# Optimization experiments

Measured on AMD Instinct MI355X. Metric: run time of the kernel, lower is better.

## Reference

```python
import jax, jax.numpy as jnp
import numpy as np

NHEAD = 16
EPS_L1 = 1e-12
LN_EPS = 1e-5


def _layernorm(x, g, b):
    mu = jnp.mean(x, axis=-1, keepdims=True)
    var = jnp.mean(jnp.square(x - mu), axis=-1, keepdims=True)
    return (x - mu) / jnp.sqrt(var + LN_EPS) * g + b


def setup_inputs() -> dict:
    key = jax.random.key(0)
    ks = jax.random.split(key, 16)
    S, B, E, P, F = 2048, 2, 1024, 64, 4096
    sc = lambda n: 1.0 / np.sqrt(n)
    return {
        "src": jax.random.normal(ks[0], (S, B, E), jnp.float32),
        "pos_embed": jax.random.normal(ks[1], (B, P, S), jnp.float32),
        "in_proj_w": jax.random.normal(ks[2], (3 * E, E), jnp.float32) * sc(E),
        "in_proj_b": jnp.zeros((3 * E,), jnp.float32),
        "out_w": jax.random.normal(ks[3], (E, E), jnp.float32) * sc(E),
        "out_b": jnp.zeros((E,), jnp.float32),
        "lin1_w": jax.random.normal(ks[4], (F, E), jnp.float32) * sc(E),
        "lin1_b": jnp.zeros((F,), jnp.float32),
        "lin2_w": jax.random.normal(ks[5], (E, F), jnp.float32) * sc(F),
        "lin2_b": jnp.zeros((E,), jnp.float32),
        "ln1_g": jnp.ones((E,), jnp.float32),
        "ln1_b": jnp.zeros((E,), jnp.float32),
        "ln2_g": jnp.ones((E,), jnp.float32),
        "ln2_b": jnp.zeros((E,), jnp.float32),
        "pos_w": jax.random.normal(ks[6], (P, P), jnp.float32) * sc(P),
        "pos_b": jnp.zeros((P,), jnp.float32),
    }


def reference(src, pos_embed, in_proj_w, in_proj_b, out_w, out_b,
              lin1_w, lin1_b, lin2_w, lin2_b,
              ln1_g, ln1_b, ln2_g, ln2_b, pos_w, pos_b):
    S, B, E = src.shape
    H = NHEAD
    Dh = E // H

    # --- custom positional-similarity kernel (cosine_similarity w/ L1 norm) ---
    pe = jnp.einsum('bps,qp->bqs', pos_embed, pos_w) + pos_b[None, :, None]  # learnable pos
    l1 = jnp.maximum(jnp.sum(jnp.abs(pe), axis=1, keepdims=True), EPS_L1)
    pe = pe / l1                                                # [B,P,S]
    pos_sim = jnp.einsum('bps,bpt->bst', pe, pe)                # [B,S,S]

    # --- manual multi-head self-attention ---
    qkv = src @ in_proj_w.T + in_proj_b                          # [S,B,3E]
    q, k, v = jnp.split(qkv, 3, axis=-1)
    q = q * (Dh ** -0.5)
    to_bhsd = lambda t: jnp.transpose(t.reshape(S, B, H, Dh), (1, 2, 0, 3))
    q, k, v = to_bhsd(q), to_bhsd(k), to_bhsd(v)                 # [B,H,S,Dh]
    scores = jnp.einsum('bhsd,bhtd->bhst', q, k) + pos_sim[:, None]
    attn = jax.nn.softmax(scores, axis=-1)                       # [B,H,S,S]
    ctx = jnp.einsum('bhst,bhtd->bhsd', attn, v)                 # [B,H,S,Dh]
    ctx = jnp.transpose(ctx, (2, 0, 1, 3)).reshape(S, B, E)
    attn_out = ctx @ out_w.T + out_b

    # --- residual + norm + FFN (post-norm, relu) ---
    x = _layernorm(src + attn_out, ln1_g, ln1_b)
    ff = jax.nn.relu(x @ lin1_w.T + lin1_b) @ lin2_w.T + lin2_b
    return _layernorm(x + ff, ln2_g, ln2_b)
```

## Files before the change

### kernel.cpp

```cpp
#include <hip/hip_runtime.h>
#include <hip/hip_bf16.h>
#include <math.h>

#define S_LEN 2048
#define BATCH 2
#define EMB   1024
#define NH    16
#define DH    64
#define E3    3072
#define FF    4096
#define PP    64
#define QSCALE 0.18033688f
#define LOG2E  1.4426950408889634f

typedef __bf16 bf16x8 __attribute__((ext_vector_type(8)));
typedef float  floatx4 __attribute__((ext_vector_type(4)));

__device__ __forceinline__ void load_lds16(const void* g, void* l) {
  __builtin_amdgcn_global_load_lds(
      (const __attribute__((address_space(1))) void*)g,
      (__attribute__((address_space(3))) void*)l, 16, 0, 0);
}

__device__ __forceinline__ float hw_exp2(float x) {
  float r;
  asm("v_exp_f32 %0, %1" : "=v"(r) : "v"(x));
  return r;
}

__global__ __launch_bounds__(256) void cvt5_kernel(
    const float* __restrict__ in0, __hip_bfloat16* __restrict__ o0,
    const float* __restrict__ in1, __hip_bfloat16* __restrict__ o1,
    const float* __restrict__ in2, __hip_bfloat16* __restrict__ o2,
    const float* __restrict__ in3, __hip_bfloat16* __restrict__ o3,
    const float* __restrict__ in4, __hip_bfloat16* __restrict__ o4)
{
  int bid = blockIdx.x;
  const float* in; __hip_bfloat16* out; int base;
  if      (bid < 2048) { in = in0; out = o0; base = bid; }
  else if (bid < 3584) { in = in1; out = o1; base = bid - 2048; }
  else if (bid < 4096) { in = in2; out = o2; base = bid - 3584; }
  else if (bid < 6144) { in = in3; out = o3; base = bid - 4096; }
  else                 { in = in4; out = o4; base = bid - 6144; }
  int i = (base * 256 + threadIdx.x) * 8;
  float4 a = *(const float4*)&in[i];
  float4 b = *(const float4*)&in[i + 4];
  __hip_bfloat16 t[8];
  t[0] = __float2bfloat16(a.x); t[1] = __float2bfloat16(a.y);
  t[2] = __float2bfloat16(a.z); t[3] = __float2bfloat16(a.w);
  t[4] = __float2bfloat16(b.x); t[5] = __float2bfloat16(b.y);
  t[6] = __float2bfloat16(b.z); t[7] = __float2bfloat16(b.w);
  *(float4*)&out[i] = *(float4*)t;
}

__global__ __launch_bounds__(64) void pe_kernel(
    const float* __restrict__ pos_embed, const float* __restrict__ pos_w,
    const float* __restrict__ pos_b, __hip_bfloat16* __restrict__ peT,
    __hip_bfloat16* __restrict__ peQ)
{
  __shared__ float pw[PP * PP];
  int tid = threadIdx.x;
  for (int i = 0; i < PP; ++i) pw[i * PP + tid] = pos_w[i * PP + tid];
  __syncthreads();
  int s = blockIdx.x * 64 + tid;
  int b = blockIdx.y;
  float acc[PP];
#pragma unroll
  for (int q = 0; q < PP; ++q) acc[q] = pos_b[q];
  for (int p = 0; p < PP; ++p) {
    float x = pos_embed[(size_t)(b * PP + p) * S_LEN + s];
#pragma unroll
    for (int q = 0; q < PP; ++q) acc[q] += pw[q * PP + p] * x;
  }
  float l1 = 0.f;
#pragma unroll
  for (int q = 0; q < PP; ++q) l1 += fabsf(acc[q]);
  float inv = 1.f / fmaxf(l1, 1e-12f);
  __hip_bfloat16 tmp[PP], tmq[PP];
#pragma unroll
  for (int q = 0; q < PP; ++q) {
    float v = acc[q] * inv;
    tmp[q] = __float2bfloat16(v);
    tmq[q] = __float2bfloat16(v * LOG2E);
  }
  float4* dst = (float4*)&peT[((size_t)b * S_LEN + s) * PP];
  float4* dsq = (float4*)&peQ[((size_t)b * S_LEN + s) * PP];
#pragma unroll
  for (int i = 0; i < 8; ++i) { dst[i] = ((float4*)tmp)[i]; dsq[i] = ((float4*)tmq)[i]; }
}

template <int WR, int WC>
__global__ __launch_bounds__(256) void gemm_bf16(
    const __hip_bfloat16* __restrict__ A, const __hip_bfloat16* __restrict__ W,
    const float* __restrict__ bias, float* __restrict__ Cf,
    __hip_bfloat16* __restrict__ Cb, int M, int N, int K, int relu, int qkscale,
    int ldA, int ldW, long strideA, long strideW, long strideC)
{
  constexpr int BM = 2 * WR * 16;
  constexpr int BN = 2 * WC * 16;
  __shared__ __bf16 As[BM * 64];
  __shared__ __bf16 Bs[BN * 64];
  A += (size_t)blockIdx.z * strideA;
  W += (size_t)blockIdx.z * strideW;
  int tid = threadIdx.x;
  int bm = blockIdx.y * BM;
  int bn = blockIdx.x * BN;
  int wave = tid >> 6, lane = tid & 63;
  int wm = (wave & 1) * (WR * 16), wn = (wave >> 1) * (WC * 16);
  int srow = tid >> 3, scb = tid & 7;
  int gcb = scb ^ (srow & 7);
  const __hip_bfloat16* Ap = A + (size_t)(bm + srow) * ldA + gcb * 8;
  const __hip_bfloat16* Wp = W + (size_t)(bn + srow) * ldW + gcb * 8;
  __bf16* AsBase = As + tid * 8;
  __bf16* BsBase = Bs + tid * 8;
  int r15 = lane & 15, quad = lane >> 4;

  floatx4 acc[WR * WC];
#pragma unroll
  for (int i = 0; i < WR * WC; ++i) acc[i] = (floatx4){0.f, 0.f, 0.f, 0.f};

  for (int k0 = 0; k0 < K; k0 += 64) {
    __syncthreads();
#pragma unroll
    for (int io = 0; io < BM / 32; ++io)
      load_lds16(Ap + (size_t)(32 * io) * ldA + k0, AsBase + io * 2048);
#pragma unroll
    for (int io = 0; io < BN / 32; ++io)
      load_lds16(Wp + (size_t)(32 * io) * ldW + k0, BsBase + io * 2048);
    __syncthreads();
#pragma unroll
    for (int kc = 0; kc < 2; ++kc) {
      bf16x8 af[WR], bfv[WC];
      int kb = kc * 4 + quad;
#pragma unroll
      for (int i = 0; i < WR; ++i) {
        int rowa = wm + i * 16 + r15;
        af[i] = *(const bf16x8*)&As[rowa * 64 + (kb ^ (rowa & 7)) * 8];
      }
#pragma unroll
      for (int j = 0; j < WC; ++j) {
        int rowb = wn + j * 16 + r15;
        bfv[j] = *(const bf16x8*)&Bs[rowb * 64 + (kb ^ (rowb & 7)) * 8];
      }
#pragma unroll
      for (int i = 0; i < WR; ++i)
#pragma unroll
        for (int j = 0; j < WC; ++j)
          acc[i * WC + j] = __builtin_amdgcn_mfma_f32_16x16x32_bf16(
              af[i], bfv[j], acc[i * WC + j], 0, 0, 0);
    }
  }
  int crow0 = bm + wm + quad * 4;
  int ccol0 = bn + wn + r15;
  float* CfB = Cf ? Cf + (long)blockIdx.z * strideC : nullptr;
  __hip_bfloat16* CbB = Cb;
#pragma unroll
  for (int j = 0; j < WC; ++j) {
    int col = ccol0 + j * 16;
    float bv = (bias && blockIdx.z == 0) ? bias[col] : 0.f;
    float scale = (qkscale && col < EMB) ? QSCALE : 1.f;
#pragma unroll
    for (int i = 0; i < WR; ++i) {
#pragma unroll
      for (int r = 0; r < 4; ++r) {
        int row = crow0 + i * 16 + r;
        float v = (acc[i * WC + j][r] + bv) * scale;
        if (relu) v = fmaxf(v, 0.f);
        if (CfB) CfB[(size_t)row * N + col] = v;
        if (CbB) CbB[(size_t)row * N + col] = __float2bfloat16(v);
      }
    }
  }
}

__global__ __launch_bounds__(512, 2) void gemm256_bf16(
    const __hip_bfloat16* __restrict__ A, const __hip_bfloat16* __restrict__ W,
    const float* __restrict__ bias, __hip_bfloat16* __restrict__ Cb,
    int M, int N, int K, int relu, int qkscale)
{
  __shared__ __bf16 As[2][16384];
  __shared__ __bf16 Bs[2][16384];
  const int tid = threadIdx.x;
  const int nwgx = gridDim.x;
  const int nwg = nwgx * gridDim.y;
  const int lin = blockIdx.y * nwgx + blockIdx.x;
  const int cpx = nwg >> 3;
  const int swz = (lin & 7) * cpx + (lin >> 3);
  const int bm = (swz / nwgx) * 256;
  const int bn = (swz % nwgx) * 256;
  const int wave = tid >> 6, lane = tid & 63;
  const int wm = (wave >> 2) * 128, wn = (wave & 3) * 64;
  const int r15 = lane & 15, quad = lane >> 4;
  const int srow = tid >> 3, scb = tid & 7;
  const int NT = K >> 6;

  const __hip_bfloat16* Ap = A + (size_t)bm * K;
  const __hip_bfloat16* Wp = W + (size_t)bn * K;

  auto stageA = [&](int buf, int k0, int h) {
#pragma unroll
    for (int io = 0; io < 2; ++io) {
      int row = h * 128 + io * 64 + srow;
      int gcb = scb ^ (row & 7);
      load_lds16(Ap + (size_t)row * K + k0 + gcb * 8,
                 &As[buf][(h * 128 + io * 64) * 64] + tid * 8);
    }
  };
  auto stageB = [&](int buf, int k0, int h) {
#pragma unroll
    for (int io = 0; io < 2; ++io) {
      int row = h * 128 + io * 64 + srow;
      int gcb = scb ^ (row & 7);
      load_lds16(Wp + (size_t)row * K + k0 + gcb * 8,
                 &Bs[buf][(h * 128 + io * 64) * 64] + tid * 8);
    }
  };

  floatx4 acc[8][4];
#pragma unroll
  for (int i = 0; i < 8; ++i)
#pragma unroll
    for (int jn = 0; jn < 4; ++jn) acc[i][jn] = (floatx4){0.f, 0.f, 0.f, 0.f};

  stageA(0, 0, 0); stageA(0, 0, 1);
  stageB(0, 0, 0); stageB(0, 0, 1);
  stageA(1, 64, 0); stageA(1, 64, 1);
  asm volatile("s_waitcnt vmcnt(4)" ::: "memory");
  __builtin_amdgcn_s_barrier();
  __builtin_amdgcn_sched_barrier(0);

#define PHASE_BAR() do { __builtin_amdgcn_sched_barrier(0); \
                         __builtin_amdgcn_s_barrier();      \
                         __builtin_amdgcn_sched_barrier(0); } while (0)

  bf16x8 af[4][2], bfr[4][2];
  for (int j = 0; j < NT; ++j) {
    const int cur = j & 1, nxt = cur ^ 1;
    const int k1 = (j + 1) << 6, k2 = (j + 2) << 6;

#pragma unroll
    for (int i = 0; i < 4; ++i) {
      int row = wm + i * 16 + r15;
#pragma unroll
      for (int kc = 0; kc < 2; ++kc)
        af[i][kc] = *(const bf16x8*)&As[cur][row * 64 + (((kc * 4 + quad) ^ (row & 7)) * 8)];
    }
#pragma unroll
    for (int jn = 0; jn < 2; ++jn) {
      int row = wn + jn * 16 + r15;
#pragma unroll
      for (int kc = 0; kc < 2; ++kc)
        bfr[jn][kc] = *(const bf16x8*)&Bs[cur][row * 64 + (((kc * 4 + quad) ^ (row & 7)) * 8)];
    }
    if (j + 1 < NT) stageB(nxt, k1, 0);
    PHASE_BAR();
    __builtin_amdgcn_s_setprio(1);
#pragma unroll
    for (int i = 0; i < 4; ++i)
#pragma unroll
      for (int jn = 0; jn < 2; ++jn)
#pragma unroll
        for (int kc = 0; kc < 2; ++kc)
          acc[i][jn] = __builtin_amdgcn_mfma_f32_16x16x32_bf16(
              af[i][kc], bfr[jn][kc], acc[i][jn], 0, 0, 0);
    __builtin_amdgcn_s_setprio(0);
    PHASE_BAR();

#pragma unroll
    for (int jn = 2; jn < 4; ++jn) {
      int row = wn + jn * 16 + r15;
#pragma unroll
      for (int kc = 0; kc < 2; ++kc)
        bfr[jn][kc] = *(const bf16x8*)&Bs[cur][row * 64 + (((kc * 4 + quad) ^ (row & 7)) * 8)];
    }
    if (j + 1 < NT) stageB(nxt, k1, 1);
    PHASE_BAR();
    __builtin_amdgcn_s_setprio(1);
#pragma unroll
    for (int i = 0; i < 4; ++i)
#pragma unroll
      for (int jn = 2; jn < 4; ++jn)
#pragma unroll
        for (int kc = 0; kc < 2; ++kc)
          acc[i][jn] = __builtin_amdgcn_mfma_f32_16x16x32_bf16(
              af[i][kc], bfr[jn][kc], acc[i][jn], 0, 0, 0);
    __builtin_amdgcn_s_setprio(0);
    PHASE_BAR();

#pragma unroll
    for (int i = 0; i < 4; ++i) {
      int row = wm + (i + 4) * 16 + r15;
#pragma unroll
      for (int kc = 0; kc < 2; ++kc)
        af[i][kc] = *(const bf16x8*)&As[cur][row * 64 + (((kc * 4 + quad) ^ (row & 7)) * 8)];
    }
    PHASE_BAR();
    __builtin_amdgcn_s_setprio(1);
#pragma unroll
    for (int i = 0; i < 4; ++i)
#pragma unroll
      for (int jn = 2; jn < 4; ++jn)
#pragma unroll
        for (int kc = 0; kc < 2; ++kc)
          acc[i + 4][jn] = __builtin_amdgcn_mfma_f32_16x16x32_bf16(
              af[i][kc], bfr[jn][kc], acc[i + 4][jn], 0, 0, 0);
    __builtin_amdgcn_s_setprio(0);
    PHASE_BAR();

    if (j + 2 < NT) { stageA(cur, k2, 0); stageA(cur, k2, 1); }
    if (j < NT - 2) asm volatile("s_waitcnt vmcnt(4)" ::: "memory");
    else            asm volatile("s_waitcnt vmcnt(0)" ::: "memory");
    PHASE_BAR();
    __builtin_amdgcn_s_setprio(1);
#pragma unroll
    for (int i = 0; i < 4; ++i)
#pragma unroll
      for (int jn = 0; jn < 2; ++jn)
#pragma unroll
        for (int kc = 0; kc < 2; ++kc)
          acc[i + 4][jn] = __builtin_amdgcn_mfma_f32_16x16x32_bf16(
              af[i][kc], bfr[jn][kc], acc[i + 4][jn], 0, 0, 0);
    __builtin_amdgcn_s_setprio(0);
    PHASE_BAR();
  }
#undef PHASE_BAR

  const int crow0 = bm + wm + quad * 4;
  const int ccol0 = bn + wn + r15;
#pragma unroll
  for (int jn = 0; jn < 4; ++jn) {
    int col = ccol0 + jn * 16;
    float bv = bias ? bias[col] : 0.f;
    float scale = (qkscale && col < EMB) ? QSCALE : 1.f;
#pragma unroll
    for (int i = 0; i < 8; ++i) {
#pragma unroll
      for (int r = 0; r < 4; ++r) {
        int row = crow0 + i * 16 + r;
        float v = (acc[i][jn][r] + bv) * scale;
        if (relu) v = fmaxf(v, 0.f);
        Cb[(size_t)row * N + col] = __float2bfloat16(v);
      }
    }
  }
}

__global__ __launch_bounds__(256) void transpose_v(
    const __hip_bfloat16* __restrict__ qkv, __hip_bfloat16* __restrict__ vT)
{
  __shared__ __hip_bfloat16 tile[64][72];
  int c0 = blockIdx.x * 64, t0 = blockIdx.y * 64, b = blockIdx.z;
  int tid = threadIdx.x;
#pragma unroll
  for (int i = 0; i < 2; ++i) {
    int k = tid * 2 + i;
    int row = k >> 3, col = (k & 7) * 8;
    float4 v = *(const float4*)&qkv[((size_t)(t0 + row) * BATCH + b) * E3 + 2 * EMB + c0 + col];
    __hip_bfloat16 tmp[8];
    *(float4*)tmp = v;
#pragma unroll
    for (int j = 0; j < 8; ++j) tile[row][col + j] = tmp[j];
  }
  __syncthreads();
#pragma unroll
  for (int i = 0; i < 2; ++i) {
    int k = tid * 2 + i;
    int crow = k >> 3, tcol = (k & 7) * 8;
    __hip_bfloat16 tmp[8];
#pragma unroll
    for (int j = 0; j < 8; ++j) tmp[j] = tile[tcol + j][crow];
    *(float4*)&vT[((size_t)(b * EMB + c0 + crow)) * S_LEN + t0 + tcol] = *(float4*)tmp;
  }
}

__global__ __launch_bounds__(512, 4) void attn_mfma(
    const __hip_bfloat16* __restrict__ qkv,
    const __hip_bfloat16* __restrict__ vT,
    const __hip_bfloat16* __restrict__ peT,
    const __hip_bfloat16* __restrict__ peQ,
    __hip_bfloat16* __restrict__ ctx)
{
  __shared__ __bf16 Ks[2][4096];
  __shared__ __bf16 Kp[2][4096];
  __shared__ __bf16 Vs[2][4096];
  __shared__ __bf16 Ps[8192];
  int tid = threadIdx.x;
  int q0 = blockIdx.x * 128, h = blockIdx.y, b = blockIdx.z;
  int w = tid >> 6, lane = tid & 63, quad = lane >> 4, r15 = lane & 15;
  int srow = tid >> 3, scb = tid & 7;
  int x7 = r15 & 7;

  const __hip_bfloat16* kbase = qkv + EMB + (size_t)h * DH;
  const __hip_bfloat16* vbase = vT + ((size_t)b * EMB + h * DH) * S_LEN;
  const __hip_bfloat16* pkbase = peT + (size_t)b * S_LEN * PP;
  const __hip_bfloat16* pqbase = peQ + (size_t)b * S_LEN * PP;

  bf16x8 qa[4];
  {
    int qrow = q0 + w * 16 + r15;
#pragma unroll
    for (int kc = 0; kc < 2; ++kc)
      qa[kc] = *(const bf16x8*)&qkv[
          ((size_t)qrow * BATCH + b) * E3 + h * DH + kc * 32 + quad * 8];
#pragma unroll
    for (int kc = 0; kc < 2; ++kc)
      qa[2 + kc] = *(const bf16x8*)&pqbase[
          (size_t)qrow * PP + kc * 32 + quad * 8];
  }

  {
    int row = srow;
    int gcb = scb ^ (row & 7);
    load_lds16(kbase + ((size_t)row * BATCH + b) * E3 + gcb * 8, Ks[0] + tid * 8);
    load_lds16(pkbase + (size_t)row * PP + gcb * 8, Kp[0] + tid * 8);
    load_lds16(vbase + (size_t)row * S_LEN + gcb * 8, Vs[0] + tid * 8);
  }
  __syncthreads();

  floatx4 of[4];
#pragma unroll
  for (int j = 0; j < 4; ++j) of[j] = (floatx4){0.f, 0.f, 0.f, 0.f};
  float lp = 0.f;

  __bf16* pw = Ps + w * 1024;

  for (int kt = 0; kt < 32; ++kt) {
    int cur = kt & 1;
    int t0 = kt * 64;
    if (kt < 31) {
      int tn = t0 + 64;
      int nb = cur ^ 1;
      int row = srow;
      int gcb = scb ^ (row & 7);
      load_lds16(kbase + ((size_t)(tn + row) * BATCH + b) * E3 + gcb * 8,
                 Ks[nb] + tid * 8);
      load_lds16(pkbase + (size_t)(tn + row) * PP + gcb * 8,
                 Kp[nb] + tid * 8);
      load_lds16(vbase + (size_t)row * S_LEN + tn + gcb * 8,
                 Vs[nb] + tid * 8);
    }

    floatx4 sf[4];
#pragma unroll
    for (int j = 0; j < 4; ++j) sf[j] = (floatx4){0.f, 0.f, 0.f, 0.f};
#pragma unroll
    for (int j = 0; j < 4; ++j) {
      int rowk = j * 16 + r15;
      int rx = rowk & 7;
      bf16x8 kf0 = *(const bf16x8*)&Ks[cur][rowk * 64 + ((quad ^ rx)) * 8];
      bf16x8 kf1 = *(const bf16x8*)&Ks[cur][rowk * 64 + (((4 + quad) ^ rx)) * 8];
      bf16x8 kp0 = *(const bf16x8*)&Kp[cur][rowk * 64 + ((quad ^ rx)) * 8];
      bf16x8 kp1 = *(const bf16x8*)&Kp[cur][rowk * 64 + (((4 + quad) ^ rx)) * 8];
      sf[j] = __builtin_amdgcn_mfma_f32_16x16x32_bf16(kf0, qa[0], sf[j], 0, 0, 0);
      sf[j] = __builtin_amdgcn_mfma_f32_16x16x32_bf16(kf1, qa[1], sf[j], 0, 0, 0);
      sf[j] = __builtin_amdgcn_mfma_f32_16x16x32_bf16(kp0, qa[2], sf[j], 0, 0, 0);
      sf[j] = __builtin_amdgcn_mfma_f32_16x16x32_bf16(kp1, qa[3], sf[j], 0, 0, 0);
    }

#pragma unroll
    for (int j = 0; j < 4; ++j) {
      float e0 = hw_exp2(sf[j][0]);
      float e1 = hw_exp2(sf[j][1]);
      float e2 = hw_exp2(sf[j][2]);
      float e3 = hw_exp2(sf[j][3]);
      lp += (e0 + e1) + (e2 + e3);
      __hip_bfloat16 t4[4];
      t4[0] = __float2bfloat16(e0); t4[1] = __float2bfloat16(e1);
      t4[2] = __float2bfloat16(e2); t4[3] = __float2bfloat16(e3);
      int addr = r15 * 64 + (((j * 2 + (quad >> 1)) ^ x7) * 8) + (quad & 1) * 4;
      *(float2*)&pw[addr] = *(float2*)t4;
    }
    __asm__ volatile("s_waitcnt lgkmcnt(0)" ::: "memory");

    bf16x8 pb0 = *(const bf16x8*)&pw[r15 * 64 + ((quad ^ x7) * 8)];
    bf16x8 pb1 = *(const bf16x8*)&pw[r15 * 64 + (((4 + quad) ^ x7) * 8)];
#pragma unroll
    for (int jd = 0; jd < 4; ++jd) {
      int rowd = jd * 16 + r15;
      bf16x8 vb0 = *(const bf16x8*)&Vs[cur][rowd * 64 + (quad ^ (rowd & 7)) * 8];
      bf16x8 vb1 = *(const bf16x8*)&Vs[cur][rowd * 64 + ((4 + quad) ^ (rowd & 7)) * 8];
      of[jd] = __builtin_amdgcn_mfma_f32_16x16x32_bf16(vb0, pb0, of[jd], 0, 0, 0);
      of[jd] = __builtin_amdgcn_mfma_f32_16x16x32_bf16(vb1, pb1, of[jd], 0, 0, 0);
    }
    __syncthreads();
  }

  {
    float l = lp;
    l += __shfl_xor(l, 16, 64);
    l += __shfl_xor(l, 32, 64);
    float inv = 1.f / l;
    size_t rbase = ((size_t)(q0 + w * 16 + r15) * BATCH + b) * EMB + h * DH;
#pragma unroll
    for (int jd = 0; jd < 4; ++jd) {
      __hip_bfloat16 o4[4];
      o4[0] = __float2bfloat16(of[jd][0] * inv);
      o4[1] = __float2bfloat16(of[jd][1] * inv);
      o4[2] = __float2bfloat16(of[jd][2] * inv);
      o4[3] = __float2bfloat16(of[jd][3] * inv);
      *(float2*)&ctx[rbase + jd * 16 + quad * 4] = *(float2*)o4;
    }
  }
}

__global__ __launch_bounds__(256) void ln_kernel(
    const float* __restrict__ x1, const float* __restrict__ x2,
    const float* __restrict__ g, const float* __restrict__ bb,
    float* __restrict__ out, __hip_bfloat16* __restrict__ out_bf)
{
  int row = blockIdx.x;
  int tid = threadIdx.x;
  const float* p1 = x1 + (size_t)row * EMB;
  const float* p2 = x2 + (size_t)row * EMB;
  float4 v1 = *(const float4*)&p1[tid * 4];
  float4 v2 = *(const float4*)&p2[tid * 4];
  float x[4] = {v1.x + v2.x, v1.y + v2.y, v1.z + v2.z, v1.w + v2.w};
  float s = x[0] + x[1] + x[2] + x[3];
  float s2 = x[0] * x[0] + x[1] * x[1] + x[2] * x[2] + x[3] * x[3];
#pragma unroll
  for (int off = 32; off >= 1; off >>= 1) {
    s  += __shfl_xor(s, off, 64);
    s2 += __shfl_xor(s2, off, 64);
  }
  __shared__ float ws1[4], ws2[4];
  int wid = tid >> 6, lane = tid & 63;
  if (lane == 0) { ws1[wid] = s; ws2[wid] = s2; }
  __syncthreads();
  s  = ws1[0] + ws1[1] + ws1[2] + ws1[3];
  s2 = ws2[0] + ws2[1] + ws2[2] + ws2[3];
  float mean = s * (1.f / EMB);
  float var  = s2 * (1.f / EMB) - mean * mean;
  float inv  = rsqrtf(var + 1e-5f);
  float4 gv = *(const float4*)&g[tid * 4];
  float4 bv = *(const float4*)&bb[tid * 4];
  float4 o;
  o.x = (x[0] - mean) * inv * gv.x + bv.x;
  o.y = (x[1] - mean) * inv * gv.y + bv.y;
  o.z = (x[2] - mean) * inv * gv.z + bv.z;
  o.w = (x[3] - mean) * inv * gv.w + bv.w;
  *(float4*)&out[(size_t)row * EMB + tid * 4] = o;
  if (out_bf) {
    __hip_bfloat16 t[4];
    t[0] = __float2bfloat16(o.x); t[1] = __float2bfloat16(o.y);
    t[2] = __float2bfloat16(o.z); t[3] = __float2bfloat16(o.w);
    *(float2*)&out_bf[(size_t)row * EMB + tid * 4] = *(float2*)t;
  }
}

__global__ __launch_bounds__(256) void ln3_kernel(
    const float* __restrict__ x1, const float* __restrict__ x2,
    const float* __restrict__ x3,
    const float* __restrict__ g, const float* __restrict__ bb,
    float* __restrict__ out)
{
  int row = blockIdx.x;
  int tid = threadIdx.x;
  const float* p1 = x1 + (size_t)row * EMB;
  const float* p2 = x2 + (size_t)row * EMB;
  const float* p3 = x3 + (size_t)row * EMB;
  float4 v1 = *(const float4*)&p1[tid * 4];
  float4 v2 = *(const float4*)&p2[tid * 4];
  float4 v3 = *(const float4*)&p3[tid * 4];
  float x[4] = {v1.x + v2.x + v3.x, v1.y + v2.y + v3.y,
                v1.z + v2.z + v3.z, v1.w + v2.w + v3.w};
  float s = x[0] + x[1] + x[2] + x[3];
  float s2 = x[0] * x[0] + x[1] * x[1] + x[2] * x[2] + x[3] * x[3];
#pragma unroll
  for (int off = 32; off >= 1; off >>= 1) {
    s  += __shfl_xor(s, off, 64);
    s2 += __shfl_xor(s2, off, 64);
  }
  __shared__ float ws1[4], ws2[4];
  int wid = tid >> 6, lane = tid & 63;
  if (lane == 0) { ws1[wid] = s; ws2[wid] = s2; }
  __syncthreads();
  s  = ws1[0] + ws1[1] + ws1[2] + ws1[3];
  s2 = ws2[0] + ws2[1] + ws2[2] + ws2[3];
  float mean = s * (1.f / EMB);
  float var  = s2 * (1.f / EMB) - mean * mean;
  float inv  = rsqrtf(var + 1e-5f);
  float4 gv = *(const float4*)&g[tid * 4];
  float4 bv = *(const float4*)&bb[tid * 4];
  float4 o;
  o.x = (x[0] - mean) * inv * gv.x + bv.x;
  o.y = (x[1] - mean) * inv * gv.y + bv.y;
  o.z = (x[2] - mean) * inv * gv.z + bv.z;
  o.w = (x[3] - mean) * inv * gv.w + bv.w;
  *(float4*)&out[(size_t)row * EMB + tid * 4] = o;
}

extern "C" void kernel_launch(void* const* d_in, const int* in_sizes, int n_in,
                              void* d_out, int out_size, void* d_ws, size_t ws_size,
                              hipStream_t stream)
{
  const float* src       = (const float*)d_in[0];
  const float* pos_embed = (const float*)d_in[1];
  const float* in_proj_w = (const float*)d_in[2];
  const float* in_proj_b = (const float*)d_in[3];
  const float* out_w     = (const float*)d_in[4];
  const float* out_b     = (const float*)d_in[5];
  const float* lin1_w    = (const float*)d_in[6];
  const float* lin1_b    = (const float*)d_in[7];
  const float* lin2_w    = (const float*)d_in[8];
  const float* lin2_b    = (const float*)d_in[9];
  const float* ln1_g     = (const float*)d_in[10];
  const float* ln1_b     = (const float*)d_in[11];
  const float* ln2_g     = (const float*)d_in[12];
  const float* ln2_b     = (const float*)d_in[13];
  const float* pos_w     = (const float*)d_in[14];
  const float* pos_b     = (const float*)d_in[15];
  float* out = (float*)d_out;
  float* ws  = (float*)d_ws;

  __hip_bfloat16* peT    = (__hip_bfloat16*)ws;
  __hip_bfloat16* peQ    = (__hip_bfloat16*)(ws + 131072);
  __hip_bfloat16* qkv_bf = (__hip_bfloat16*)(ws + 8519680);
  __hip_bfloat16* vT_bf  = (__hip_bfloat16*)(ws + 14811136);
  __hip_bfloat16* src_bf = (__hip_bfloat16*)(ws + 16908288);
  __hip_bfloat16* inw_bf  = (__hip_bfloat16*)(ws + 19005440);
  __hip_bfloat16* outw_bf = (__hip_bfloat16*)(ws + 20578304);
  __hip_bfloat16* ctx_bf = (__hip_bfloat16*)(ws + 21102592);
  __hip_bfloat16* l1w_bf = (__hip_bfloat16*)(ws + 23199744);
  __hip_bfloat16* l2w_bf = (__hip_bfloat16*)(ws + 25296896);
  float* proj            = ws + 27394048;
  __hip_bfloat16* x_bf   = (__hip_bfloat16*)ws;
  float* xbuf            = ws + 2097152;
  __hip_bfloat16* h1_bf  = (__hip_bfloat16*)(ws + 6291456);
  float* proj2           = ws + 14811136;

  const int M = S_LEN * BATCH;

  cvt5_kernel<<<8192, 256, 0, stream>>>(
      src, src_bf, in_proj_w, inw_bf, out_w, outw_bf,
      lin1_w, l1w_bf, lin2_w, l2w_bf);
  pe_kernel<<<dim3(S_LEN / 64, BATCH), 64, 0, stream>>>(pos_embed, pos_w, pos_b, peT, peQ);
  gemm256_bf16<<<dim3(E3 / 256, M / 256), 512, 0, stream>>>(
      src_bf, inw_bf, in_proj_b, qkv_bf, M, E3, EMB, 0, 1);
  transpose_v<<<dim3(EMB / 64, S_LEN / 64, BATCH), 256, 0, stream>>>(qkv_bf, vT_bf);
  attn_mfma<<<dim3(S_LEN / 128, NH, BATCH), 512, 0, stream>>>(
      qkv_bf, vT_bf, peT, peQ, ctx_bf);
  gemm_bf16<2, 4><<<dim3(EMB / 128, M / 64, 1), 256, 0, stream>>>(
      ctx_bf, outw_bf, out_b, proj, nullptr, M, EMB, EMB, 0, 0, EMB, EMB, 0, 0, 0);
  ln_kernel<<<dim3(M), 256, 0, stream>>>(src, proj, ln1_g, ln1_b, xbuf, x_bf);
  gemm256_bf16<<<dim3(FF / 256, M / 256), 512, 0, stream>>>(
      x_bf, l1w_bf, lin1_b, h1_bf, M, FF, EMB, 1, 0);
  gemm_bf16<4, 4><<<dim3(EMB / 128, M / 128, 2), 256, 0, stream>>>(
      h1_bf, l2w_bf, lin2_b, proj, nullptr, M, EMB, FF / 2, 0, 0,
      FF, FF, FF / 2, FF / 2, (long)(proj2 - proj));
  ln3_kernel<<<dim3(M), 256, 0, stream>>>(xbuf, proj, proj2, ln2_g, ln2_b, out);
}
```

Baseline: 398.8 us.

## Run FFN down-projection on 256-tile GEMM with 4-way split-K atomic accumulation

The second FFN GEMM moves from the 128x128 generic GEMM with 2-way split-K into separate buffers onto the 256x256 pipelined GEMM, using a 4-way split-K over the z grid. Partial sums are accumulated with fp32 atomicAdd into a buffer that the first layernorm kernel zeroes. The final layernorm now reads two inputs instead of three. This is meant to use the faster large-tile GEMM and drop one partial-buffer read, at the cost of atomic traffic and reduced determinism from the order of float additions.

```diff
diff --git a/kernel.cpp b/kernel.cpp
--- a/kernel.cpp
+++ b/kernel.cpp
@@ -176,7 +176,8 @@
 __global__ __launch_bounds__(512, 2) void gemm256_bf16(
     const __hip_bfloat16* __restrict__ A, const __hip_bfloat16* __restrict__ W,
     const float* __restrict__ bias, __hip_bfloat16* __restrict__ Cb,
-    int M, int N, int K, int relu, int qkscale)
+    int M, int N, int K, int relu, int qkscale,
+    int ldA, int ldW, long zsA, long zsW, float* __restrict__ Cfat)
 {
   __shared__ __bf16 As[2][16384];
   __shared__ __bf16 Bs[2][16384];
@@ -194,15 +195,17 @@
   const int srow = tid >> 3, scb = tid & 7;
   const int NT = K >> 6;
 
-  const __hip_bfloat16* Ap = A + (size_t)bm * K;
-  const __hip_bfloat16* Wp = W + (size_t)bn * K;
+  A += (size_t)blockIdx.z * zsA;
+  W += (size_t)blockIdx.z * zsW;
+  const __hip_bfloat16* Ap = A + (size_t)bm * ldA;
+  const __hip_bfloat16* Wp = W + (size_t)bn * ldW;
 
   auto stageA = [&](int buf, int k0, int h) {
 #pragma unroll
     for (int io = 0; io < 2; ++io) {
       int row = h * 128 + io * 64 + srow;
       int gcb = scb ^ (row & 7);
-      load_lds16(Ap + (size_t)row * K + k0 + gcb * 8,
+      load_lds16(Ap + (size_t)row * ldA + k0 + gcb * 8,
                  &As[buf][(h * 128 + io * 64) * 64] + tid * 8);
     }
   };
@@ -211,7 +214,7 @@
     for (int io = 0; io < 2; ++io) {
       int row = h * 128 + io * 64 + srow;
       int gcb = scb ^ (row & 7);
-      load_lds16(Wp + (size_t)row * K + k0 + gcb * 8,
+      load_lds16(Wp + (size_t)row * ldW + k0 + gcb * 8,
                  &Bs[buf][(h * 128 + io * 64) * 64] + tid * 8);
     }
   };
@@ -330,7 +333,7 @@
 #pragma unroll
   for (int jn = 0; jn < 4; ++jn) {
     int col = ccol0 + jn * 16;
-    float bv = bias ? bias[col] : 0.f;
+    float bv = (bias && blockIdx.z == 0) ? bias[col] : 0.f;
     float scale = (qkscale && col < EMB) ? QSCALE : 1.f;
 #pragma unroll
     for (int i = 0; i < 8; ++i) {
@@ -339,7 +342,8 @@
         int row = crow0 + i * 16 + r;
         float v = (acc[i][jn][r] + bv) * scale;
         if (relu) v = fmaxf(v, 0.f);
-        Cb[(size_t)row * N + col] = __float2bfloat16(v);
+        if (Cfat) atomicAdd(&Cfat[(size_t)row * N + col], v);
+        else      Cb[(size_t)row * N + col] = __float2bfloat16(v);
       }
     }
   }
@@ -506,7 +510,8 @@
 __global__ __launch_bounds__(256) void ln_kernel(
     const float* __restrict__ x1, const float* __restrict__ x2,
     const float* __restrict__ g, const float* __restrict__ bb,
-    float* __restrict__ out, __hip_bfloat16* __restrict__ out_bf)
+    float* __restrict__ out, __hip_bfloat16* __restrict__ out_bf,
+    float* __restrict__ zero_out)
 {
   int row = blockIdx.x;
   int tid = threadIdx.x;
@@ -545,48 +550,10 @@
     t[2] = __float2bfloat16(o.z); t[3] = __float2bfloat16(o.w);
     *(float2*)&out_bf[(size_t)row * EMB + tid * 4] = *(float2*)t;
   }
-}
-
-__global__ __launch_bounds__(256) void ln3_kernel(
-    const float* __restrict__ x1, const float* __restrict__ x2,
-    const float* __restrict__ x3,
-    const float* __restrict__ g, const float* __restrict__ bb,
-    float* __restrict__ out)
-{
-  int row = blockIdx.x;
-  int tid = threadIdx.x;
-  const float* p1 = x1 + (size_t)row * EMB;
-  const float* p2 = x2 + (size_t)row * EMB;
-  const float* p3 = x3 + (size_t)row * EMB;
-  float4 v1 = *(const float4*)&p1[tid * 4];
-  float4 v2 = *(const float4*)&p2[tid * 4];
-  float4 v3 = *(const float4*)&p3[tid * 4];
-  float x[4] = {v1.x + v2.x + v3.x, v1.y + v2.y + v3.y,
-                v1.z + v2.z + v3.z, v1.w + v2.w + v3.w};
-  float s = x[0] + x[1] + x[2] + x[3];
-  float s2 = x[0] * x[0] + x[1] * x[1] + x[2] * x[2] + x[3] * x[3];
-#pragma unroll
-  for (int off = 32; off >= 1; off >>= 1) {
-    s  += __shfl_xor(s, off, 64);
-    s2 += __shfl_xor(s2, off, 64);
-  }
-  __shared__ float ws1[4], ws2[4];
-  int wid = tid >> 6, lane = tid & 63;
-  if (lane == 0) { ws1[wid] = s; ws2[wid] = s2; }
-  __syncthreads();
-  s  = ws1[0] + ws1[1] + ws1[2] + ws1[3];
-  s2 = ws2[0] + ws2[1] + ws2[2] + ws2[3];
-  float mean = s * (1.f / EMB);
-  float var  = s2 * (1.f / EMB) - mean * mean;
-  float inv  = rsqrtf(var + 1e-5f);
-  float4 gv = *(const float4*)&g[tid * 4];
-  float4 bv = *(const float4*)&bb[tid * 4];
-  float4 o;
-  o.x = (x[0] - mean) * inv * gv.x + bv.x;
-  o.y = (x[1] - mean) * inv * gv.y + bv.y;
-  o.z = (x[2] - mean) * inv * gv.z + bv.z;
-  o.w = (x[3] - mean) * inv * gv.w + bv.w;
-  *(float4*)&out[(size_t)row * EMB + tid * 4] = o;
+  if (zero_out) {
+    float4 z = {0.f, 0.f, 0.f, 0.f};
+    *(float4*)&zero_out[(size_t)row * EMB + tid * 4] = z;
+  }
 }
 
 extern "C" void kernel_launch(void* const* d_in, const int* in_sizes, int n_in,
@@ -626,7 +593,6 @@
   __hip_bfloat16* x_bf   = (__hip_bfloat16*)ws;
   float* xbuf            = ws + 2097152;
   __hip_bfloat16* h1_bf  = (__hip_bfloat16*)(ws + 6291456);
-  float* proj2           = ws + 14811136;
 
   const int M = S_LEN * BATCH;
 
@@ -635,17 +601,19 @@
       lin1_w, l1w_bf, lin2_w, l2w_bf);
   pe_kernel<<<dim3(S_LEN / 64, BATCH), 64, 0, stream>>>(pos_embed, pos_w, pos_b, peT, peQ);
   gemm256_bf16<<<dim3(E3 / 256, M / 256), 512, 0, stream>>>(
-      src_bf, inw_bf, in_proj_b, qkv_bf, M, E3, EMB, 0, 1);
+      src_bf, inw_bf, in_proj_b, qkv_bf, M, E3, EMB, 0, 1,
+      EMB, EMB, 0, 0, nullptr);
   transpose_v<<<dim3(EMB / 64, S_LEN / 64, BATCH), 256, 0, stream>>>(qkv_bf, vT_bf);
   attn_mfma<<<dim3(S_LEN / 128, NH, BATCH), 512, 0, stream>>>(
       qkv_bf, vT_bf, peT, peQ, ctx_bf);
   gemm_bf16<2, 4><<<dim3(EMB / 128, M / 64, 1), 256, 0, stream>>>(
       ctx_bf, outw_bf, out_b, proj, nullptr, M, EMB, EMB, 0, 0, EMB, EMB, 0, 0, 0);
-  ln_kernel<<<dim3(M), 256, 0, stream>>>(src, proj, ln1_g, ln1_b, xbuf, x_bf);
+  ln_kernel<<<dim3(M), 256, 0, stream>>>(src, proj, ln1_g, ln1_b, xbuf, x_bf, proj);
   gemm256_bf16<<<dim3(FF / 256, M / 256), 512, 0, stream>>>(
-      x_bf, l1w_bf, lin1_b, h1_bf, M, FF, EMB, 1, 0);
-  gemm_bf16<4, 4><<<dim3(EMB / 128, M / 128, 2), 256, 0, stream>>>(
-      h1_bf, l2w_bf, lin2_b, proj, nullptr, M, EMB, FF / 2, 0, 0,
-      FF, FF, FF / 2, FF / 2, (long)(proj2 - proj));
-  ln3_kernel<<<dim3(M), 256, 0, stream>>>(xbuf, proj, proj2, ln2_g, ln2_b, out);
-}
+      x_bf, l1w_bf, lin1_b, h1_bf, M, FF, EMB, 1, 0,
+      EMB, EMB, 0, 0, nullptr);
+  gemm256_bf16<<<dim3(EMB / 256, M / 256, 4), 512, 0, stream>>>(
+      h1_bf, l2w_bf, lin2_b, nullptr, M, EMB, FF / 4, 0, 0,
+      FF, FF, (long)(FF / 4), (long)(FF / 4), proj);
+  ln_kernel<<<dim3(M), 256, 0, stream>>>(xbuf, proj, ln2_g, ln2_b, out, nullptr, nullptr);
+}
```

Measured after the change: 430.1 us. +7.8%, slower.
